# Performance work log

Measured on AMD Instinct MI355X. Metric: run time of the kernel, lower is better.

The kernel has to match this reference:

```python
import jax, jax.numpy as jnp
import numpy as np

N = 10000
E = 640000


def setup_inputs() -> dict:
    key = jax.random.key(0)
    k = jax.random.split(key, 6)
    x = jax.random.normal(k[0], (N, 128), dtype=jnp.float32)
    edge_index = jax.random.randint(k[1], (2, E), 0, N, dtype=jnp.int64)
    # Linear weights stored as [in, out] (torch stores [out, in]; math is x @ W.T + b)
    w1 = jax.random.normal(k[2], (128, 128), dtype=jnp.float32) * 0.05
    b1 = jax.random.normal(k[3], (128,), dtype=jnp.float32) * 0.05
    w2 = jax.random.normal(k[4], (128, 128), dtype=jnp.float32) * 0.05
    b2 = jax.random.normal(k[5], (128,), dtype=jnp.float32) * 0.05
    return {"x": x, "edge_index": edge_index, "w1": w1, "b1": b1, "w2": w2, "b2": b2}


def gin_conv(x, src, dst, w, b, eps=0.0):
    # aggregate: out[i] = sum over edges (src->dst=i) of x[src]
    agg = jax.ops.segment_sum(x[src], dst, num_segments=N)  # [N, d]
    h = (1.0 + eps) * x + agg
    return h @ w + b


def reference(x, edge_index, w1, b1, w2, b2):
    src, dst = edge_index[0], edge_index[1]
    h = gin_conv(x, src, dst, w1, b1)
    h = jax.nn.relu(h)
    h = gin_conv(h, src, dst, w2, b2)
    return jax.nn.log_softmax(h, axis=1)
```

## Files before the change

kernel.cpp:

```cpp
#include <hip/hip_runtime.h>
#include <cstdint>

#define NNODES 10000
#define FDIM 128
#define MAXDEG 192
#define SLOTS 48

typedef _Float16 h2v  __attribute__((ext_vector_type(2)));
typedef _Float16 f16x8 __attribute__((ext_vector_type(8)));
typedef float    f32x4 __attribute__((ext_vector_type(4)));

__device__ __align__(16)  int      g_cnt[NNODES * 4];
__device__                int      g_bucket[NNODES * MAXDEG];
__device__ __align__(256) unsigned g_xh [(NNODES + 1) * FDIM / 2];
__device__ __align__(256) unsigned g_h1h[(NNODES + 1) * FDIM / 2];
__device__ __align__(16)  unsigned g_wf[2 * 8192];

__device__ inline h2v as_h2(unsigned u) { return __builtin_bit_cast(h2v, u); }
__device__ inline unsigned as_u(h2v v) { return __builtin_bit_cast(unsigned, v); }
__device__ inline unsigned pack_f16x2(float a, float b) {
  h2v v; v[0] = (_Float16)a; v[1] = (_Float16)b;
  return as_u(v);
}
__device__ inline void vadd4(uint4& a, const uint4& b) {
  a.x = as_u(as_h2(a.x) + as_h2(b.x));
  a.y = as_u(as_h2(a.y) + as_h2(b.y));
  a.z = as_u(as_h2(a.z) + as_h2(b.z));
  a.w = as_u(as_h2(a.w) + as_h2(b.w));
}

__global__ __launch_bounds__(256) void prep_kernel(
    const float* __restrict__ x, const int* __restrict__ ei,
    const float* __restrict__ w1, const float* __restrict__ w2,
    int E_, int EBLK, int CBLK) {
  const int bid = blockIdx.x;
  if (bid < EBLK) {
    int e = bid * 256 + threadIdx.x;
    if (e < E_) {
      int d = ei[E_ + e];
      int s = ei[e];
      int st = e & 3;
      int p = atomicAdd(&g_cnt[d * 4 + st], 1);
      if (p < SLOTS) g_bucket[d * MAXDEG + st * SLOTS + p] = s;
    }
  } else if (bid < EBLK + CBLK) {
    int i = (bid - EBLK) * 256 + threadIdx.x;
    if (i < NNODES * 32) {
      float4 v = *(const float4*)(x + 4 * (size_t)i);
      uint2 o; o.x = pack_f16x2(v.x, v.y); o.y = pack_f16x2(v.z, v.w);
      *(uint2*)(g_xh + 2 * (size_t)i) = o;
    }
  } else {
    int idx = (bid - EBLK - CBLK) * 256 + threadIdx.x;
    const float* w = (idx >= 2048) ? w2 : w1;
    int s = idx & 2047;
    int sl = s & 63, nk = s >> 6;
    int n = nk >> 2, kc = nk & 3;
    int kbase = kc * 32 + (sl >> 4) * 8;
    int f = n * 16 + (sl & 15);
    unsigned d0 = pack_f16x2(w[(size_t)(kbase + 0) * FDIM + f],
                             w[(size_t)(kbase + 1) * FDIM + f]);
    unsigned d1 = pack_f16x2(w[(size_t)(kbase + 2) * FDIM + f],
                             w[(size_t)(kbase + 3) * FDIM + f]);
    unsigned d2 = pack_f16x2(w[(size_t)(kbase + 4) * FDIM + f],
                             w[(size_t)(kbase + 5) * FDIM + f]);
    unsigned d3 = pack_f16x2(w[(size_t)(kbase + 6) * FDIM + f],
                             w[(size_t)(kbase + 7) * FDIM + f]);
    *(uint4*)(g_wf + (idx >> 11) * 8192 + 4 * s) = make_uint4(d0, d1, d2, d3);
  }
}

template <int MODE>
__global__ __launch_bounds__(512) void gin_layer_kernel(
    const float* __restrict__ bvec,
    float* __restrict__ out_g) {
  const unsigned* __restrict__ xh = (MODE == 0) ? g_xh : g_h1h;

  __shared__ __align__(16) unsigned al[16 * 68];
  __shared__ __align__(16) unsigned cfu[16 * 132];

  const int tid = threadIdx.x;
  const int wave = tid >> 6, lane = tid & 63;
  const int quad = lane >> 4, m16 = lane & 15;
  const int node0 = blockIdx.x * 16;

  uint4 bf[4];
  {
    const unsigned* wfp = g_wf + (MODE ? 8192 : 0);
#pragma unroll
    for (int kc = 0; kc < 4; ++kc)
      bf[kc] = *(const uint4*)(wfp + ((wave * 4 + kc) * 64 + lane) * 4);
  }
  const float bb = bvec[wave * 16 + m16];

  const int myn0 = node0 + wave * 2;
  uint4 self4[2];
  int o1[2], o2[2], o3[2], dgg[2];
#pragma unroll
  for (int i = 0; i < 2; ++i) {
    self4[i] = *(const uint4*)(xh + (size_t)(myn0 + i) * 64 + (m16 << 2));
    int4 c = *(const int4*)(g_cnt + (myn0 + i) * 4);
    int a = (c.x > SLOTS) ? SLOTS : c.x;
    int bq = (c.y > SLOTS) ? SLOTS : c.y;
    int cq = (c.z > SLOTS) ? SLOTS : c.z;
    int dq = (c.w > SLOTS) ? SLOTS : c.w;
    o1[i] = a; o2[i] = a + bq; o3[i] = a + bq + cq; dgg[i] = a + bq + cq + dq;
  }

  for (int i = 0; i < 2; ++i) {
    h2v a0 = as_h2(0u), a1 = as_h2(0u), a2 = as_h2(0u), a3 = as_h2(0u);
    const int deg = dgg[i];
    const int* nb = g_bucket + (size_t)(myn0 + i) * MAXDEG;
    for (int p = 0; p < deg; p += 64) {
      int n = deg - p; if (n > 64) n = 64;
      int myedge = NNODES;
      if (lane < n) {
        int g = p + lane;
        int base = 0;
        if (g >= o1[i]) base = o1[i];
        if (g >= o2[i]) base = o2[i];
        if (g >= o3[i]) base = o3[i];
        int st = (g >= o1[i]) + (g >= o2[i]) + (g >= o3[i]);
        myedge = nb[st * SLOTS + (g - base)];
      }
      const int nst = (n + 3) >> 2;
      int s = 0;
      for (; s + 8 <= nst; s += 8) {
        uint4 t[8];
#pragma unroll
        for (int k = 0; k < 8; ++k) {
          int e = __builtin_amdgcn_ds_bpermute((((s + k) << 2) | quad) << 2, myedge);
          t[k] = *(const uint4*)(xh + (unsigned)((e << 6) | (m16 << 2)));
        }
#pragma unroll
        for (int st2 = 1; st2 < 8; st2 <<= 1)
#pragma unroll
          for (int k = 0; k < 8; k += 2 * st2) vadd4(t[k], t[k + st2]);
        a0 += as_h2(t[0].x); a1 += as_h2(t[0].y);
        a2 += as_h2(t[0].z); a3 += as_h2(t[0].w);
      }
      if (s + 4 <= nst) {
        uint4 t[4];
#pragma unroll
        for (int k = 0; k < 4; ++k) {
          int e = __builtin_amdgcn_ds_bpermute((((s + k) << 2) | quad) << 2, myedge);
          t[k] = *(const uint4*)(xh + (unsigned)((e << 6) | (m16 << 2)));
        }
        vadd4(t[0], t[1]); vadd4(t[2], t[3]); vadd4(t[0], t[2]);
        a0 += as_h2(t[0].x); a1 += as_h2(t[0].y);
        a2 += as_h2(t[0].z); a3 += as_h2(t[0].w);
        s += 4;
      }
      for (; s < nst; ++s) {
        int e = __builtin_amdgcn_ds_bpermute(((s << 2) | quad) << 2, myedge);
        uint4 t = *(const uint4*)(xh + (unsigned)((e << 6) | (m16 << 2)));
        a0 += as_h2(t.x); a1 += as_h2(t.y); a2 += as_h2(t.z); a3 += as_h2(t.w);
      }
    }
    int r;
    r = __shfl_xor((int)as_u(a0), 16, 64); a0 += as_h2((unsigned)r);
    r = __shfl_xor((int)as_u(a0), 32, 64); a0 += as_h2((unsigned)r);
    r = __shfl_xor((int)as_u(a1), 16, 64); a1 += as_h2((unsigned)r);
    r = __shfl_xor((int)as_u(a1), 32, 64); a1 += as_h2((unsigned)r);
    r = __shfl_xor((int)as_u(a2), 16, 64); a2 += as_h2((unsigned)r);
    r = __shfl_xor((int)as_u(a2), 32, 64); a2 += as_h2((unsigned)r);
    r = __shfl_xor((int)as_u(a3), 16, 64); a3 += as_h2((unsigned)r);
    r = __shfl_xor((int)as_u(a3), 32, 64); a3 += as_h2((unsigned)r);
    a0 += as_h2(self4[i].x); a1 += as_h2(self4[i].y);
    a2 += as_h2(self4[i].z); a3 += as_h2(self4[i].w);
    if (quad == 0)
      *(uint4*)(al + (wave * 2 + i) * 68 + (m16 << 2)) =
          make_uint4(as_u(a0), as_u(a1), as_u(a2), as_u(a3));
  }
  __syncthreads();

  uint4 af[4];
#pragma unroll
  for (int kc = 0; kc < 4; ++kc)
    af[kc] = *(const uint4*)(al + m16 * 68 + kc * 16 + quad * 4);

  const int n = wave;
  f32x4 acc = {0.f, 0.f, 0.f, 0.f};
#pragma unroll
  for (int kc = 0; kc < 4; ++kc)
    acc = __builtin_amdgcn_mfma_f32_16x16x32_f16(
            __builtin_bit_cast(f16x8, af[kc]),
            __builtin_bit_cast(f16x8, bf[kc]), acc, 0, 0, 0);

  if (MODE == 0) {
    _Float16* ch = (_Float16*)cfu;
    const int f = n * 16 + m16;
#pragma unroll
    for (int reg = 0; reg < 4; ++reg)
      ch[(quad * 4 + reg) * 136 + f] = (_Float16)fmaxf(acc[reg] + bb, 0.f);
    __syncthreads();
    const int row = tid >> 5, c2 = (tid & 31) * 2;
    uint2 v = *(const uint2*)(cfu + row * 68 + c2);
    *(uint2*)(&g_h1h[(size_t)(node0 + row) * 64 + c2]) = v;
  } else {
    float* cf = (float*)cfu;
    const int f = n * 16 + m16;
#pragma unroll
    for (int reg = 0; reg < 4; ++reg)
      cf[(quad * 4 + reg) * 132 + f] = acc[reg] + bb;
    __syncthreads();
    const int row = tid >> 5, li = tid & 31;
    const float* base = cf + row * 132 + li * 4;
    float4 a4 = *(const float4*)(base);
    float mx = fmaxf(fmaxf(a4.x, a4.y), fmaxf(a4.z, a4.w));
#pragma unroll
    for (int off = 16; off >= 1; off >>= 1)
      mx = fmaxf(mx, __shfl_xor(mx, off, 64));
    float s = (__expf(a4.x - mx) + __expf(a4.y - mx))
            + (__expf(a4.z - mx) + __expf(a4.w - mx));
#pragma unroll
    for (int off = 16; off >= 1; off >>= 1)
      s += __shfl_xor(s, off, 64);
    const float ls = mx + __logf(s);
    float* orow = out_g + (size_t)(node0 + row) * FDIM + li * 4;
    *(float4*)(orow) = make_float4(a4.x - ls, a4.y - ls, a4.z - ls, a4.w - ls);
    if (tid < 64) g_cnt[node0 * 4 + tid] = 0;
  }
}

extern "C" void kernel_launch(void* const* d_in, const int* in_sizes, int n_in,
                              void* d_out, int out_size, void* d_ws, size_t ws_size,
                              hipStream_t stream) {
  const float* x  = (const float*)d_in[0];
  const int*   ei = (const int*)d_in[1];
  const float* w1 = (const float*)d_in[2];
  const float* b1 = (const float*)d_in[3];
  const float* w2 = (const float*)d_in[4];
  const float* b2 = (const float*)d_in[5];
  float* out = (float*)d_out;

  const int E_ = in_sizes[1] / 2;
  const int EBLK = (E_ + 255) / 256;
  const int CBLK = (NNODES * 32 + 255) / 256;
  const int WBLK = 16;

  prep_kernel<<<EBLK + CBLK + WBLK, 256, 0, stream>>>(x, ei, w1, w2, E_, EBLK, CBLK);

  gin_layer_kernel<0><<<625, 512, 0, stream>>>(b1, nullptr);
  gin_layer_kernel<1><<<625, 512, 0, stream>>>(b2, out);
}
```

Measured before the change: 127.9 us.

## Assign one node per wave with 8-node blocks and preloaded edge indices

Each block now handles 8 nodes instead of 16, and each wave aggregates a single node instead of two in sequence, doubling the grid to 1250 blocks. All of a node's edge indices (up to 192) are loaded up front into three registers per lane. The gather then runs in uniform batches of 32 edges, padded with a dummy zero row, so the 8/4/1 tail-loop variants are gone. The aim is more parallelism and memory-level parallelism in the latency-bound gather. The cost is half the MFMA rows going unused in the 16-row tile, extra padding loads, and block-level work (weight fragment loads, syncs) repeated twice as often.

```diff
diff --git a/kernel.cpp b/kernel.cpp
--- a/kernel.cpp
+++ b/kernel.cpp
@@ -77,12 +77,13 @@
   const unsigned* __restrict__ xh = (MODE == 0) ? g_xh : g_h1h;
 
   __shared__ __align__(16) unsigned al[16 * 68];
-  __shared__ __align__(16) unsigned cfu[16 * 132];
+  __shared__ __align__(16) unsigned cfu[8 * 132];
 
   const int tid = threadIdx.x;
   const int wave = tid >> 6, lane = tid & 63;
   const int quad = lane >> 4, m16 = lane & 15;
-  const int node0 = blockIdx.x * 16;
+  const int node0 = blockIdx.x * 8;
+  const int myn = node0 + wave;
 
   uint4 bf[4];
   {
@@ -93,85 +94,71 @@
   }
   const float bb = bvec[wave * 16 + m16];
 
-  const int myn0 = node0 + wave * 2;
-  uint4 self4[2];
-  int o1[2], o2[2], o3[2], dgg[2];
-#pragma unroll
-  for (int i = 0; i < 2; ++i) {
-    self4[i] = *(const uint4*)(xh + (size_t)(myn0 + i) * 64 + (m16 << 2));
-    int4 c = *(const int4*)(g_cnt + (myn0 + i) * 4);
+  for (int i2 = tid; i2 < 8 * 68; i2 += 512) al[8 * 68 + i2] = 0;
+
+  uint4 self4 = *(const uint4*)(xh + (size_t)myn * 64 + (m16 << 2));
+  int o1, o2, o3, deg;
+  {
+    int4 c = *(const int4*)(g_cnt + myn * 4);
     int a = (c.x > SLOTS) ? SLOTS : c.x;
     int bq = (c.y > SLOTS) ? SLOTS : c.y;
     int cq = (c.z > SLOTS) ? SLOTS : c.z;
     int dq = (c.w > SLOTS) ? SLOTS : c.w;
-    o1[i] = a; o2[i] = a + bq; o3[i] = a + bq + cq; dgg[i] = a + bq + cq + dq;
-  }
-
-  for (int i = 0; i < 2; ++i) {
-    h2v a0 = as_h2(0u), a1 = as_h2(0u), a2 = as_h2(0u), a3 = as_h2(0u);
-    const int deg = dgg[i];
-    const int* nb = g_bucket + (size_t)(myn0 + i) * MAXDEG;
-    for (int p = 0; p < deg; p += 64) {
-      int n = deg - p; if (n > 64) n = 64;
-      int myedge = NNODES;
-      if (lane < n) {
-        int g = p + lane;
-        int base = 0;
-        if (g >= o1[i]) base = o1[i];
-        if (g >= o2[i]) base = o2[i];
-        if (g >= o3[i]) base = o3[i];
-        int st = (g >= o1[i]) + (g >= o2[i]) + (g >= o3[i]);
-        myedge = nb[st * SLOTS + (g - base)];
-      }
-      const int nst = (n + 3) >> 2;
-      int s = 0;
-      for (; s + 8 <= nst; s += 8) {
-        uint4 t[8];
-#pragma unroll
-        for (int k = 0; k < 8; ++k) {
-          int e = __builtin_amdgcn_ds_bpermute((((s + k) << 2) | quad) << 2, myedge);
-          t[k] = *(const uint4*)(xh + (unsigned)((e << 6) | (m16 << 2)));
-        }
-#pragma unroll
-        for (int st2 = 1; st2 < 8; st2 <<= 1)
-#pragma unroll
-          for (int k = 0; k < 8; k += 2 * st2) vadd4(t[k], t[k + st2]);
-        a0 += as_h2(t[0].x); a1 += as_h2(t[0].y);
-        a2 += as_h2(t[0].z); a3 += as_h2(t[0].w);
-      }
-      if (s + 4 <= nst) {
-        uint4 t[4];
-#pragma unroll
-        for (int k = 0; k < 4; ++k) {
-          int e = __builtin_amdgcn_ds_bpermute((((s + k) << 2) | quad) << 2, myedge);
-          t[k] = *(const uint4*)(xh + (unsigned)((e << 6) | (m16 << 2)));
-        }
-        vadd4(t[0], t[1]); vadd4(t[2], t[3]); vadd4(t[0], t[2]);
-        a0 += as_h2(t[0].x); a1 += as_h2(t[0].y);
-        a2 += as_h2(t[0].z); a3 += as_h2(t[0].w);
-        s += 4;
-      }
-      for (; s < nst; ++s) {
-        int e = __builtin_amdgcn_ds_bpermute(((s << 2) | quad) << 2, myedge);
-        uint4 t = *(const uint4*)(xh + (unsigned)((e << 6) | (m16 << 2)));
-        a0 += as_h2(t.x); a1 += as_h2(t.y); a2 += as_h2(t.z); a3 += as_h2(t.w);
-      }
-    }
-    int r;
-    r = __shfl_xor((int)as_u(a0), 16, 64); a0 += as_h2((unsigned)r);
-    r = __shfl_xor((int)as_u(a0), 32, 64); a0 += as_h2((unsigned)r);
-    r = __shfl_xor((int)as_u(a1), 16, 64); a1 += as_h2((unsigned)r);
-    r = __shfl_xor((int)as_u(a1), 32, 64); a1 += as_h2((unsigned)r);
-    r = __shfl_xor((int)as_u(a2), 16, 64); a2 += as_h2((unsigned)r);
-    r = __shfl_xor((int)as_u(a2), 32, 64); a2 += as_h2((unsigned)r);
-    r = __shfl_xor((int)as_u(a3), 16, 64); a3 += as_h2((unsigned)r);
-    r = __shfl_xor((int)as_u(a3), 32, 64); a3 += as_h2((unsigned)r);
-    a0 += as_h2(self4[i].x); a1 += as_h2(self4[i].y);
-    a2 += as_h2(self4[i].z); a3 += as_h2(self4[i].w);
-    if (quad == 0)
-      *(uint4*)(al + (wave * 2 + i) * 68 + (m16 << 2)) =
-          make_uint4(as_u(a0), as_u(a1), as_u(a2), as_u(a3));
-  }
+    o1 = a; o2 = a + bq; o3 = a + bq + cq; deg = a + bq + cq + dq;
+  }
+
+  const int* nb = g_bucket + (size_t)myn * MAXDEG;
+  int idxr[3];
+#pragma unroll
+  for (int r = 0; r < 3; ++r) {
+    int g = r * 64 + lane;
+    int e = NNODES;
+    if (g < deg) {
+      int base = 0;
+      if (g >= o1) base = o1;
+      if (g >= o2) base = o2;
+      if (g >= o3) base = o3;
+      int st = (g >= o1) + (g >= o2) + (g >= o3);
+      e = nb[st * SLOTS + (g - base)];
+    }
+    idxr[r] = e;
+  }
+
+  h2v a0 = as_h2(0u), a1 = as_h2(0u), a2 = as_h2(0u), a3 = as_h2(0u);
+  const int nbat = (deg + 31) >> 5;
+  for (int bt = 0; bt < nbat; ++bt) {
+    const int s0 = bt << 3;
+    const int r = s0 >> 4;
+    const int src = (r == 0) ? idxr[0] : ((r == 1) ? idxr[1] : idxr[2]);
+    uint4 t[8];
+#pragma unroll
+    for (int k = 0; k < 8; ++k) {
+      int e = __builtin_amdgcn_ds_bpermute(
+          (((((s0 + k) & 15) << 2) | quad) << 2), src);
+      t[k] = *(const uint4*)(xh + (unsigned)((e << 6) | (m16 << 2)));
+    }
+#pragma unroll
+    for (int st2 = 1; st2 < 8; st2 <<= 1)
+#pragma unroll
+      for (int k = 0; k < 8; k += 2 * st2) vadd4(t[k], t[k + st2]);
+    a0 += as_h2(t[0].x); a1 += as_h2(t[0].y);
+    a2 += as_h2(t[0].z); a3 += as_h2(t[0].w);
+  }
+
+  int rr;
+  rr = __shfl_xor((int)as_u(a0), 16, 64); a0 += as_h2((unsigned)rr);
+  rr = __shfl_xor((int)as_u(a0), 32, 64); a0 += as_h2((unsigned)rr);
+  rr = __shfl_xor((int)as_u(a1), 16, 64); a1 += as_h2((unsigned)rr);
+  rr = __shfl_xor((int)as_u(a1), 32, 64); a1 += as_h2((unsigned)rr);
+  rr = __shfl_xor((int)as_u(a2), 16, 64); a2 += as_h2((unsigned)rr);
+  rr = __shfl_xor((int)as_u(a2), 32, 64); a2 += as_h2((unsigned)rr);
+  rr = __shfl_xor((int)as_u(a3), 16, 64); a3 += as_h2((unsigned)rr);
+  rr = __shfl_xor((int)as_u(a3), 32, 64); a3 += as_h2((unsigned)rr);
+  a0 += as_h2(self4.x); a1 += as_h2(self4.y);
+  a2 += as_h2(self4.z); a3 += as_h2(self4.w);
+  if (quad == 0)
+    *(uint4*)(al + wave * 68 + (m16 << 2)) =
+        make_uint4(as_u(a0), as_u(a1), as_u(a2), as_u(a3));
   __syncthreads();
 
   uint4 af[4];
@@ -190,36 +177,44 @@
   if (MODE == 0) {
     _Float16* ch = (_Float16*)cfu;
     const int f = n * 16 + m16;
-#pragma unroll
-    for (int reg = 0; reg < 4; ++reg)
-      ch[(quad * 4 + reg) * 136 + f] = (_Float16)fmaxf(acc[reg] + bb, 0.f);
+    if (quad < 2) {
+#pragma unroll
+      for (int reg = 0; reg < 4; ++reg)
+        ch[(quad * 4 + reg) * 136 + f] = (_Float16)fmaxf(acc[reg] + bb, 0.f);
+    }
     __syncthreads();
-    const int row = tid >> 5, c2 = (tid & 31) * 2;
-    uint2 v = *(const uint2*)(cfu + row * 68 + c2);
-    *(uint2*)(&g_h1h[(size_t)(node0 + row) * 64 + c2]) = v;
+    if (tid < 256) {
+      const int row = tid >> 5, c2 = (tid & 31) * 2;
+      uint2 v = *(const uint2*)(cfu + row * 68 + c2);
+      *(uint2*)(&g_h1h[(size_t)(node0 + row) * 64 + c2]) = v;
+    }
   } else {
     float* cf = (float*)cfu;
     const int f = n * 16 + m16;
-#pragma unroll
-    for (int reg = 0; reg < 4; ++reg)
-      cf[(quad * 4 + reg) * 132 + f] = acc[reg] + bb;
+    if (quad < 2) {
+#pragma unroll
+      for (int reg = 0; reg < 4; ++reg)
+        cf[(quad * 4 + reg) * 132 + f] = acc[reg] + bb;
+    }
     __syncthreads();
-    const int row = tid >> 5, li = tid & 31;
-    const float* base = cf + row * 132 + li * 4;
-    float4 a4 = *(const float4*)(base);
-    float mx = fmaxf(fmaxf(a4.x, a4.y), fmaxf(a4.z, a4.w));
-#pragma unroll
-    for (int off = 16; off >= 1; off >>= 1)
-      mx = fmaxf(mx, __shfl_xor(mx, off, 64));
-    float s = (__expf(a4.x - mx) + __expf(a4.y - mx))
-            + (__expf(a4.z - mx) + __expf(a4.w - mx));
-#pragma unroll
-    for (int off = 16; off >= 1; off >>= 1)
-      s += __shfl_xor(s, off, 64);
-    const float ls = mx + __logf(s);
-    float* orow = out_g + (size_t)(node0 + row) * FDIM + li * 4;
-    *(float4*)(orow) = make_float4(a4.x - ls, a4.y - ls, a4.z - ls, a4.w - ls);
-    if (tid < 64) g_cnt[node0 * 4 + tid] = 0;
+    if (tid < 256) {
+      const int row = tid >> 5, li = tid & 31;
+      const float* base = cf + row * 132 + li * 4;
+      float4 a4 = *(const float4*)(base);
+      float mx = fmaxf(fmaxf(a4.x, a4.y), fmaxf(a4.z, a4.w));
+#pragma unroll
+      for (int off = 16; off >= 1; off >>= 1)
+        mx = fmaxf(mx, __shfl_xor(mx, off, 64));
+      float s = (__expf(a4.x - mx) + __expf(a4.y - mx))
+              + (__expf(a4.z - mx) + __expf(a4.w - mx));
+#pragma unroll
+      for (int off = 16; off >= 1; off >>= 1)
+        s += __shfl_xor(s, off, 64);
+      const float ls = mx + __logf(s);
+      float* orow = out_g + (size_t)(node0 + row) * FDIM + li * 4;
+      *(float4*)(orow) = make_float4(a4.x - ls, a4.y - ls, a4.z - ls, a4.w - ls);
+    }
+    if (tid < 32) g_cnt[node0 * 4 + tid] = 0;
   }
 }
 
@@ -241,6 +236,6 @@
 
   prep_kernel<<<EBLK + CBLK + WBLK, 256, 0, stream>>>(x, ei, w1, w2, E_, EBLK, CBLK);
 
-  gin_layer_kernel<0><<<625, 512, 0, stream>>>(b1, nullptr);
-  gin_layer_kernel<1><<<625, 512, 0, stream>>>(b2, out);
-}
+  gin_layer_kernel<0><<<1250, 512, 0, stream>>>(b1, nullptr);
+  gin_layer_kernel<1><<<1250, 512, 0, stream>>>(b2, out);
+}
```

Measured after the change: 124.2 us. 2.9% less time.
